# Kernel optimization log

Hardware: AMD Instinct MI355X
Metric: run time of the kernel (lower is better)

## Reference

```python
import jax, jax.numpy as jnp
import numpy as np

ND, NS, H = 100000, 10000, 128
EDD, EDS, ESD = 600000, 600000, 600000


def setup_inputs() -> dict:
    key = jax.random.key(0)
    ks = jax.random.split(key, 32)

    def n(i, shape, s=1.0):
        return jax.random.normal(ks[i], shape, dtype=jnp.float32) * s

    inp = {
        "x_drug": n(0, (ND, H)),
        "x_se": n(1, (NS, H)),
        # edge_index[0] = source node ids, edge_index[1] = destination node ids
        "ei_dd": jnp.stack([jax.random.randint(ks[2], (EDD,), 0, ND),
                             jax.random.randint(ks[3], (EDD,), 0, ND)]),
        "ei_ds": jnp.stack([jax.random.randint(ks[4], (EDS,), 0, ND),
                             jax.random.randint(ks[5], (EDS,), 0, NS)]),
        "ei_sd": jnp.stack([jax.random.randint(ks[6], (ESD,), 0, NS),
                             jax.random.randint(ks[7], (ESD,), 0, ND)]),
    }
    i = 8
    for layer in (1, 2):
        for rel in ("dd", "ds", "sd"):
            inp[f"w{layer}_{rel}_rel"] = n(i, (H, H), 0.05); i += 1
            inp[f"b{layer}_{rel}"] = jnp.zeros((H,), jnp.float32)
            inp[f"w{layer}_{rel}_root"] = n(i, (H, H), 0.05); i += 1
    inp["bn_gamma"] = jnp.ones((H,), jnp.float32)
    inp["bn_beta"] = jnp.zeros((H,), jnp.float32)
    return inp


def _gconv(x_src, x_dst, ei, w_rel, b_rel, w_root):
    # PyG GraphConv (aggr='add'): lin_rel(sum_j x_j) + lin_root(x_dst)
    agg = jax.ops.segment_sum(x_src[ei[0]], ei[1], num_segments=x_dst.shape[0])
    return agg @ w_rel.T + b_rel + x_dst @ w_root.T


def _bn(x, gamma, beta, eps=1e-5):
    # training-mode BatchNorm1d: batch stats, biased variance
    m = x.mean(axis=0)
    v = jnp.mean((x - m) ** 2, axis=0)
    return (x - m) / jnp.sqrt(v + eps) * gamma + beta


def reference(x_drug, x_se, ei_dd, ei_ds, ei_sd,
              w1_dd_rel, b1_dd, w1_dd_root,
              w1_ds_rel, b1_ds, w1_ds_root,
              w1_sd_rel, b1_sd, w1_sd_root,
              w2_dd_rel, b2_dd, w2_dd_root,
              w2_ds_rel, b2_ds, w2_ds_root,
              w2_sd_rel, b2_sd, w2_sd_root,
              bn_gamma, bn_beta):
    lrelu = jax.nn.leaky_relu  # slope 0.01, matches F.leaky_relu default
    # layer 1: HeteroConv sums per destination type
    d1 = lrelu(_gconv(x_drug, x_drug, ei_dd, w1_dd_rel, b1_dd, w1_dd_root)
               + _gconv(x_se, x_drug, ei_sd, w1_sd_rel, b1_sd, w1_sd_root))
    s1 = lrelu(_gconv(x_drug, x_se, ei_ds, w1_ds_rel, b1_ds, w1_ds_root))
    # layer 2
    d2 = lrelu(_gconv(d1, d1, ei_dd, w2_dd_rel, b2_dd, w2_dd_root)
               + _gconv(s1, d1, ei_sd, w2_sd_rel, b2_sd, w2_sd_root))
    s2 = lrelu(_gconv(d1, s1, ei_ds, w2_ds_rel, b2_ds, w2_ds_root))
    # shared BatchNorm applied per node type
    return _bn(d2, bn_gamma, bn_beta), _bn(s2, bn_gamma, bn_beta)
```

## Files before the change

### kernel.cpp

```cpp
#include <hip/hip_runtime.h>
#include <hip/hip_bf16.h>

#define H 128
#define ND 100000
#define NS 10000
#define CAPD 32
#define CAPS 128

typedef __attribute__((ext_vector_type(8))) _Float16 f16x8;
typedef __attribute__((ext_vector_type(4))) float f32x4;

__device__ inline ushort f2h(float f) {
    union { _Float16 h; ushort u; } c; c.h = (_Float16)f; return c.u;
}
__device__ inline float h2f(ushort u) {
    union { ushort u; _Float16 h; } c; c.u = u; return (float)c.h;
}

__global__ __launch_bounds__(256) void f2h_all(
    const float* __restrict__ xd, const float* __restrict__ xs,
    ushort* __restrict__ od, ushort* __restrict__ os)
{
    int i = blockIdx.x * 256 + threadIdx.x;
    const int nD = ND * H / 4;
    const int nT = (ND + NS) * H / 4;
    if (i >= nT) return;
    const float* in; ushort* out; int j;
    if (i < nD) { in = xd; out = od; j = i; }
    else        { in = xs; out = os; j = i - nD; }
    float4 v = reinterpret_cast<const float4*>(in)[j];
    ushort4 o;
    o.x = f2h(v.x); o.y = f2h(v.y); o.z = f2h(v.z); o.w = f2h(v.w);
    reinterpret_cast<ushort4*>(out)[j] = o;
}

__global__ void prep_weights(
    const float* w1ddr, const float* w1ddo, const float* w1sdr, const float* w1sdo,
    const float* w1dsr, const float* w1dso,
    const float* w2ddr, const float* w2ddo, const float* w2sdr, const float* w2sdo,
    const float* w2dsr, const float* w2dso,
    const float* b1dd, const float* b1sd, const float* b1ds,
    const float* b2dd, const float* b2sd, const float* b2ds,
    ushort* Wd1, ushort* Ws1, ushort* Wd2, ushort* Ws2, float* bias)
{
    int i = blockIdx.x * blockDim.x + threadIdx.x;
    if (i < 16384) {
        Wd1[i]           = f2h(w1ddr[i]);
        Wd1[16384 + i]   = f2h(w1sdr[i]);
        Wd1[32768 + i]   = f2h(w1ddo[i] + w1sdo[i]);
        Ws1[i]           = f2h(w1dsr[i]);
        Ws1[16384 + i]   = f2h(w1dso[i]);
        Wd2[i]           = f2h(w2ddr[i]);
        Wd2[16384 + i]   = f2h(w2sdr[i]);
        Wd2[32768 + i]   = f2h(w2ddo[i] + w2sdo[i]);
        Ws2[i]           = f2h(w2dsr[i]);
        Ws2[16384 + i]   = f2h(w2dso[i]);
    }
    if (i < H) {
        bias[i]         = b1dd[i] + b1sd[i];
        bias[H + i]     = b1ds[i];
        bias[2*H + i]   = b2dd[i] + b2sd[i];
        bias[3*H + i]   = b2ds[i];
    }
}

__global__ __launch_bounds__(256) void fill3(
    const int* __restrict__ s1, const int* __restrict__ d1, int E1, int n1, int* __restrict__ c1, int* __restrict__ o1,
    const int* __restrict__ s2, const int* __restrict__ d2, int E2, int n2, int* __restrict__ c2, ushort* __restrict__ o2,
    const int* __restrict__ s3, const int* __restrict__ d3, int E3, int n3, int* __restrict__ c3, int* __restrict__ o3,
    int g1, int g2)
{
    int pass = blockIdx.x & 7;
    int b = blockIdx.x >> 3;
    int rel;
    const int *es, *ed; int *cur; int E, n;
    if (b < g1)           { es = s1; ed = d1; cur = c1; E = E1; n = n1; rel = 0; }
    else if (b < g1 + g2) { es = s2; ed = d2; cur = c2; E = E2; n = n2; rel = 1; b -= g1; }
    else                  { es = s3; ed = d3; cur = c3; E = E3; n = n3; rel = 2; b -= g1 + g2; }
    int e = b * 256 + threadIdx.x;
    if (e >= E) return;
    int dst = ed[e];
    int lo = pass * (n >> 3);
    if (dst >= lo && dst < lo + (n >> 3)) {
        int pos = atomicAdd(&cur[dst], 1);
        if (rel == 0)      { if (pos < CAPD) o1[(size_t)dst * CAPD + pos] = es[e]; }
        else if (rel == 1) { if (pos < CAPD) o2[(size_t)dst * CAPD + pos] = (ushort)es[e]; }
        else               { if (pos < CAPS) o3[(size_t)dst * CAPS + pos] = es[e]; }
    }
}

template<typename IT>
__device__ inline uint4 agg_row(const ushort* __restrict__ src,
                                const IT* __restrict__ si, int cnt, int c)
{
    float a0 = 0.f, a1 = 0.f, a2 = 0.f, a3 = 0.f;
    float a4 = 0.f, a5 = 0.f, a6 = 0.f, a7 = 0.f;
    int p = 0;
    for (; p + 4 <= cnt; p += 4) {
        int s0 = (int)si[p], s1 = (int)si[p + 1], s2 = (int)si[p + 2], s3 = (int)si[p + 3];
        uint4 v0 = *reinterpret_cast<const uint4*>(src + (size_t)s0 * H + c * 8);
        uint4 v1 = *reinterpret_cast<const uint4*>(src + (size_t)s1 * H + c * 8);
        uint4 v2 = *reinterpret_cast<const uint4*>(src + (size_t)s2 * H + c * 8);
        uint4 v3 = *reinterpret_cast<const uint4*>(src + (size_t)s3 * H + c * 8);
        a0 += h2f((ushort)(v0.x & 0xffff)) + h2f((ushort)(v1.x & 0xffff))
            + h2f((ushort)(v2.x & 0xffff)) + h2f((ushort)(v3.x & 0xffff));
        a1 += h2f((ushort)(v0.x >> 16))    + h2f((ushort)(v1.x >> 16))
            + h2f((ushort)(v2.x >> 16))    + h2f((ushort)(v3.x >> 16));
        a2 += h2f((ushort)(v0.y & 0xffff)) + h2f((ushort)(v1.y & 0xffff))
            + h2f((ushort)(v2.y & 0xffff)) + h2f((ushort)(v3.y & 0xffff));
        a3 += h2f((ushort)(v0.y >> 16))    + h2f((ushort)(v1.y >> 16))
            + h2f((ushort)(v2.y >> 16))    + h2f((ushort)(v3.y >> 16));
        a4 += h2f((ushort)(v0.z & 0xffff)) + h2f((ushort)(v1.z & 0xffff))
            + h2f((ushort)(v2.z & 0xffff)) + h2f((ushort)(v3.z & 0xffff));
        a5 += h2f((ushort)(v0.z >> 16))    + h2f((ushort)(v1.z >> 16))
            + h2f((ushort)(v2.z >> 16))    + h2f((ushort)(v3.z >> 16));
        a6 += h2f((ushort)(v0.w & 0xffff)) + h2f((ushort)(v1.w & 0xffff))
            + h2f((ushort)(v2.w & 0xffff)) + h2f((ushort)(v3.w & 0xffff));
        a7 += h2f((ushort)(v0.w >> 16))    + h2f((ushort)(v1.w >> 16))
            + h2f((ushort)(v2.w >> 16))    + h2f((ushort)(v3.w >> 16));
    }
    for (; p < cnt; ++p) {
        int s0 = (int)si[p];
        uint4 v0 = *reinterpret_cast<const uint4*>(src + (size_t)s0 * H + c * 8);
        a0 += h2f((ushort)(v0.x & 0xffff));
        a1 += h2f((ushort)(v0.x >> 16));
        a2 += h2f((ushort)(v0.y & 0xffff));
        a3 += h2f((ushort)(v0.y >> 16));
        a4 += h2f((ushort)(v0.z & 0xffff));
        a5 += h2f((ushort)(v0.z >> 16));
        a6 += h2f((ushort)(v0.w & 0xffff));
        a7 += h2f((ushort)(v0.w >> 16));
    }
    uint4 o;
    o.x = (uint)f2h(a0) | ((uint)f2h(a1) << 16);
    o.y = (uint)f2h(a2) | ((uint)f2h(a3) << 16);
    o.z = (uint)f2h(a4) | ((uint)f2h(a5) << 16);
    o.w = (uint)f2h(a6) | ((uint)f2h(a7) << 16);
    return o;
}

__global__ __launch_bounds__(256) void agg3(
    const ushort* __restrict__ dtab, const ushort* __restrict__ stab,
    const int* __restrict__ cnt_dd, const int* __restrict__ si_dd, ushort* __restrict__ segdd,
    const int* __restrict__ cnt_sd, const ushort* __restrict__ si_sd, ushort* __restrict__ segsd,
    const int* __restrict__ cnt_ds, const int* __restrict__ si_ds, ushort* __restrict__ segds,
    int gA)
{
    int b = blockIdx.x;
    int rel; ushort* dst; int Ndst;
    if (b < gA)          { rel = 0; dst = segdd; Ndst = ND; }
    else if (b < 2 * gA) { rel = 1; dst = segsd; Ndst = ND; b -= gA; }
    else                 { rel = 2; dst = segds; Ndst = NS; b -= 2 * gA; }
    int d = b * 16 + (threadIdx.x >> 4);
    if (d >= Ndst) return;
    int c = threadIdx.x & 15;
    uint4 o;
    if (rel == 0) {
        int n = min(cnt_dd[d], CAPD);
        o = agg_row(dtab, si_dd + (size_t)d * CAPD, n, c);
    } else if (rel == 1) {
        int n = min(cnt_sd[d], CAPD);
        o = agg_row(stab, si_sd + (size_t)d * CAPD, n, c);
    } else {
        int n = min(cnt_ds[d], CAPS);
        o = agg_row(dtab, si_ds + (size_t)d * CAPS, n, c);
    }
    *reinterpret_cast<uint4*>(dst + (size_t)d * H + c * 8) = o;
}

template<bool OUTF32>
__global__ __launch_bounds__(256) void gemm_layer(
    const ushort* __restrict__ segdd, const ushort* __restrict__ segsd,
    const ushort* __restrict__ rootd, const ushort* __restrict__ Wd,
    const float* __restrict__ biasd, void* __restrict__ outd,
    const ushort* __restrict__ segds, const ushort* __restrict__ roots,
    const ushort* __restrict__ Ws, const float* __restrict__ biass,
    void* __restrict__ outs, float* __restrict__ sm, int GD)
{
    __shared__ union {
        struct { ushort Al[64][72]; ushort Bl[128][72]; } s;
        float red[2][16][128];
    } u;

    int b = blockIdx.x;
    const ushort *src0, *src1, *src2, *W; const float* bias; void* out;
    int M, nsrc, soff;
    if (b < GD) {
        src0 = segdd; src1 = segsd; src2 = rootd; W = Wd; bias = biasd;
        out = outd; M = ND; nsrc = 3; soff = 0;
    } else {
        b -= GD;
        src0 = segds; src1 = roots; src2 = nullptr; W = Ws; bias = biass;
        out = outs; M = NS; nsrc = 2; soff = 256;
    }

    const int t = threadIdx.x;
    const int wave = t >> 6;
    const int lane = t & 63;
    const int l15 = lane & 15;
    const int kreg = lane >> 4;
    const int block_row = b * 64;

    f32x4 acc[8] = {};

    for (int slot = 0; slot < nsrc; ++slot) {
        const ushort* sb = (slot == 0) ? src0 : (slot == 1) ? src1 : src2;
        #pragma unroll
        for (int half = 0; half < 2; ++half) {
            const int kc = half * 64;
            __syncthreads();
            #pragma unroll
            for (int it = 0; it < 2; ++it) {
                int c = t + it * 256;
                int row = c >> 3, part = c & 7;
                int grow = block_row + row;
                uint4 v = make_uint4(0, 0, 0, 0);
                if (grow < M)
                    v = *reinterpret_cast<const uint4*>(sb + (size_t)grow * H + kc + part * 8);
                *reinterpret_cast<uint4*>(&u.s.Al[row][part * 8]) = v;
            }
            #pragma unroll
            for (int it = 0; it < 4; ++it) {
                int c = t + it * 256;
                int row = c >> 3, part = c & 7;
                uint4 v = *reinterpret_cast<const uint4*>(W + slot * 16384 + row * 128 + kc + part * 8);
                *reinterpret_cast<uint4*>(&u.s.Bl[row][part * 8]) = v;
            }
            __syncthreads();

            #pragma unroll
            for (int kk = 0; kk < 2; ++kk) {
                f16x8 a = *reinterpret_cast<const f16x8*>(&u.s.Al[wave * 16 + l15][kk * 32 + kreg * 8]);
                #pragma unroll
                for (int n = 0; n < 8; ++n) {
                    f16x8 bb = *reinterpret_cast<const f16x8*>(&u.s.Bl[n * 16 + l15][kk * 32 + kreg * 8]);
                    acc[n] = __builtin_amdgcn_mfma_f32_16x16x32_f16(a, bb, acc[n], 0, 0, 0);
                }
            }
        }
    }

    float psum[8], psq[8];
    const int rb = block_row + wave * 16 + kreg * 4;
    #pragma unroll
    for (int n = 0; n < 8; ++n) {
        int col = n * 16 + l15;
        float bv = bias[col];
        float s = 0.f, q = 0.f;
        #pragma unroll
        for (int r = 0; r < 4; ++r) {
            int row = rb + r;
            if (row < M) {
                float v = acc[n][r] + bv;
                v = (v > 0.f) ? v : 0.01f * v;
                if (OUTF32) ((float*)out)[(size_t)row * H + col] = v;
                else        ((ushort*)out)[(size_t)row * H + col] = f2h(v);
                s += v; q += v * v;
            }
        }
        psum[n] = s; psq[n] = q;
    }

    if (OUTF32) {
        __syncthreads();
        const int w4k = wave * 4 + kreg;
        #pragma unroll
        for (int n = 0; n < 8; ++n) {
            int col = n * 16 + l15;
            u.red[0][w4k][col] = psum[n];
            u.red[1][w4k][col] = psq[n];
        }
        __syncthreads();
        if (t < 128) {
            float a = 0.f, q = 0.f;
            #pragma unroll
            for (int k = 0; k < 16; ++k) { a += u.red[0][k][t]; q += u.red[1][k][t]; }
            float* dstp = sm + (blockIdx.x & 7) * 512 + soff;
            atomicAdd(&dstp[t], a);
            atomicAdd(&dstp[H + t], q);
        }
    }
}

__global__ void bn_fold(const float* __restrict__ sm, float* __restrict__ stats)
{
    int t = blockIdx.x * 256 + threadIdx.x;
    float s = 0.f;
    #pragma unroll
    for (int k = 0; k < 8; ++k) s += sm[k * 512 + t];
    stats[t] = s;
}

__global__ __launch_bounds__(256) void bn_apply_all(
    float* __restrict__ d2, float* __restrict__ s2,
    const float* __restrict__ stats,
    const float* __restrict__ gamma, const float* __restrict__ beta)
{
    size_t i = (size_t)blockIdx.x * 256 + threadIdx.x;
    const size_t totD = (size_t)ND * (H / 4);
    const size_t totAll = totD + (size_t)NS * (H / 4);
    if (i >= totAll) return;
    float* x;
    const float* st;
    float inv_m;
    size_t j;
    if (i < totD) { x = d2; st = stats;       inv_m = 1.0f / ND; j = i; }
    else          { x = s2; st = stats + 256; inv_m = 1.0f / NS; j = i - totD; }
    int c4 = (int)(j & (H / 4 - 1)) * 4;
    float4 v = reinterpret_cast<float4*>(x)[j];
    float* vp = &v.x;
    #pragma unroll
    for (int k = 0; k < 4; ++k) {
        int c = c4 + k;
        float mean = st[c] * inv_m;
        float var = st[H + c] * inv_m - mean * mean;
        float sc = gamma[c] * rsqrtf(fmaxf(var, 0.f) + 1e-5f);
        vp[k] = (vp[k] - mean) * sc + beta[c];
    }
    reinterpret_cast<float4*>(x)[j] = v;
}

extern "C" void kernel_launch(void* const* d_in, const int* in_sizes, int n_in,
                              void* d_out, int out_size, void* d_ws, size_t ws_size,
                              hipStream_t stream)
{
    (void)n_in; (void)out_size; (void)ws_size;
    const float* x_drug = (const float*)d_in[0];
    const float* x_se   = (const float*)d_in[1];
    const int* ei_dd = (const int*)d_in[2];
    const int* ei_ds = (const int*)d_in[3];
    const int* ei_sd = (const int*)d_in[4];
    const int EDD = in_sizes[2] / 2;
    const int EDS = in_sizes[3] / 2;
    const int ESD = in_sizes[4] / 2;

    const float* w1_dd_rel  = (const float*)d_in[5];
    const float* b1_dd      = (const float*)d_in[6];
    const float* w1_dd_root = (const float*)d_in[7];
    const float* w1_ds_rel  = (const float*)d_in[8];
    const float* b1_ds      = (const float*)d_in[9];
    const float* w1_ds_root = (const float*)d_in[10];
    const float* w1_sd_rel  = (const float*)d_in[11];
    const float* b1_sd      = (const float*)d_in[12];
    const float* w1_sd_root = (const float*)d_in[13];
    const float* w2_dd_rel  = (const float*)d_in[14];
    const float* b2_dd      = (const float*)d_in[15];
    const float* w2_dd_root = (const float*)d_in[16];
    const float* w2_ds_rel  = (const float*)d_in[17];
    const float* b2_ds      = (const float*)d_in[18];
    const float* w2_ds_root = (const float*)d_in[19];
    const float* w2_sd_rel  = (const float*)d_in[20];
    const float* b2_sd      = (const float*)d_in[21];
    const float* w2_sd_root = (const float*)d_in[22];
    const float* gamma      = (const float*)d_in[23];
    const float* beta       = (const float*)d_in[24];

    ushort* xd_h  = (ushort*)d_ws;
    ushort* xs_h  = xd_h + (size_t)ND * H;
    ushort* segdd = xs_h + (size_t)NS * H;
    ushort* segsd = segdd + (size_t)ND * H;
    ushort* segds = segsd + (size_t)ND * H;
    ushort* Wd1 = segds + (size_t)NS * H;
    ushort* Ws1 = Wd1 + 3 * 16384;
    ushort* Wd2 = Ws1 + 2 * 16384;
    ushort* Ws2 = Wd2 + 3 * 16384;
    float* bias  = (float*)(Ws2 + 2 * 16384);
    float* stats = bias + 512;
    float* sm    = stats + 512;
    int* cnt_dd  = (int*)(sm + 8 * 512);
    int* cnt_sd  = cnt_dd + ND;
    int* cnt_ds  = cnt_sd + ND;
    int* si_dd   = cnt_ds + NS;
    int* si_ds   = si_dd + (size_t)ND * CAPD;
    ushort* si_sd = (ushort*)(si_ds + (size_t)NS * CAPS);

    ushort* d1h = xd_h;
    ushort* s1h = xs_h;

    float* d2 = (float*)d_out;
    float* s2 = d2 + (size_t)ND * H;

    hipMemsetAsync(sm, 0, ((size_t)8 * 512 + (size_t)(2 * ND + NS)) * sizeof(int), stream);

    prep_weights<<<64, 256, 0, stream>>>(
        w1_dd_rel, w1_dd_root, w1_sd_rel, w1_sd_root, w1_ds_rel, w1_ds_root,
        w2_dd_rel, w2_dd_root, w2_sd_rel, w2_sd_root, w2_ds_rel, w2_ds_root,
        b1_dd, b1_sd, b1_ds, b2_dd, b2_sd, b2_ds,
        Wd1, Ws1, Wd2, Ws2, bias);

    f2h_all<<<((ND + NS) * H / 4 + 255) / 256, 256, 0, stream>>>(x_drug, x_se, xd_h, xs_h);

    const int gDD = (EDD + 255) / 256, gSD = (ESD + 255) / 256, gDS = (EDS + 255) / 256;
    fill3<<<8 * (gDD + gSD + gDS), 256, 0, stream>>>(
        ei_dd, ei_dd + EDD, EDD, ND, cnt_dd, si_dd,
        ei_sd, ei_sd + ESD, ESD, ND, cnt_sd, si_sd,
        ei_ds, ei_ds + EDS, EDS, NS, cnt_ds, si_ds, gDD, gSD);

    const int gA = (ND + 15) / 16, gB = (NS + 15) / 16;
    const int GD = (ND + 63) / 64, GS = (NS + 63) / 64;

    agg3<<<2 * gA + gB, 256, 0, stream>>>(
        xd_h, xs_h,
        cnt_dd, si_dd, segdd,
        cnt_sd, si_sd, segsd,
        cnt_ds, si_ds, segds, gA);
    gemm_layer<false><<<GD + GS, 256, 0, stream>>>(
        segdd, segsd, xd_h, Wd1, bias, d1h,
        segds, xs_h, Ws1, bias + H, s1h, sm, GD);

    agg3<<<2 * gA + gB, 256, 0, stream>>>(
        d1h, s1h,
        cnt_dd, si_dd, segdd,
        cnt_sd, si_sd, segsd,
        cnt_ds, si_ds, segds, gA);
    gemm_layer<true><<<GD + GS, 256, 0, stream>>>(
        segdd, segsd, d1h, Wd2, bias + 2 * H, d2,
        segds, s1h, Ws2, bias + 3 * H, s2, sm, GD);

    bn_fold<<<2, 256, 0, stream>>>(sm, stats);
    bn_apply_all<<<((ND + NS) * (H / 4) + 255) / 256, 256, 0, stream>>>(d2, s2, stats, gamma, beta);
}
```

Before: 404.7 us.

## Load GEMM A operands directly into registers and fuse f2h into edge fill

The GEMM kernel stops staging the activation tile in LDS: each lane loads its own A fragments straight from global memory, and only the weight tile still goes through shared memory. This removes A-tile LDS traffic and shrinks shared memory use. The fp32-to-fp16 conversion kernel is merged into the CSR fill kernel to save one launch, and the aggregation tail loop is unrolled by two. The direct A loads drop the bounds check on the row index, so the last partial blocks read past M, which relies on the neighbouring buffer being mapped.

Result: faster. 377.1 us (-6.8%).

```diff
diff --git a/kernel.cpp b/kernel.cpp
--- a/kernel.cpp
+++ b/kernel.cpp
@@ -15,23 +15,6 @@
 }
 __device__ inline float h2f(ushort u) {
     union { ushort u; _Float16 h; } c; c.u = u; return (float)c.h;
-}
-
-__global__ __launch_bounds__(256) void f2h_all(
-    const float* __restrict__ xd, const float* __restrict__ xs,
-    ushort* __restrict__ od, ushort* __restrict__ os)
-{
-    int i = blockIdx.x * 256 + threadIdx.x;
-    const int nD = ND * H / 4;
-    const int nT = (ND + NS) * H / 4;
-    if (i >= nT) return;
-    const float* in; ushort* out; int j;
-    if (i < nD) { in = xd; out = od; j = i; }
-    else        { in = xs; out = os; j = i - nD; }
-    float4 v = reinterpret_cast<const float4*>(in)[j];
-    ushort4 o;
-    o.x = f2h(v.x); o.y = f2h(v.y); o.z = f2h(v.z); o.w = f2h(v.w);
-    reinterpret_cast<ushort4*>(out)[j] = o;
 }
 
 __global__ void prep_weights(
@@ -64,14 +47,30 @@
     }
 }
 
-__global__ __launch_bounds__(256) void fill3(
+__global__ __launch_bounds__(256) void fill_f2h(
+    const float* __restrict__ xd, const float* __restrict__ xs,
+    ushort* __restrict__ od, ushort* __restrict__ os, int F,
     const int* __restrict__ s1, const int* __restrict__ d1, int E1, int n1, int* __restrict__ c1, int* __restrict__ o1,
     const int* __restrict__ s2, const int* __restrict__ d2, int E2, int n2, int* __restrict__ c2, ushort* __restrict__ o2,
     const int* __restrict__ s3, const int* __restrict__ d3, int E3, int n3, int* __restrict__ c3, int* __restrict__ o3,
     int g1, int g2)
 {
+    if (blockIdx.x < F) {
+        int i = blockIdx.x * 256 + threadIdx.x;
+        const int nD = ND * H / 4;
+        const int nT = (ND + NS) * H / 4;
+        if (i >= nT) return;
+        const float* in; ushort* out; int j;
+        if (i < nD) { in = xd; out = od; j = i; }
+        else        { in = xs; out = os; j = i - nD; }
+        float4 v = reinterpret_cast<const float4*>(in)[j];
+        ushort4 o;
+        o.x = f2h(v.x); o.y = f2h(v.y); o.z = f2h(v.z); o.w = f2h(v.w);
+        reinterpret_cast<ushort4*>(out)[j] = o;
+        return;
+    }
     int pass = blockIdx.x & 7;
-    int b = blockIdx.x >> 3;
+    int b = (blockIdx.x - F) >> 3;
     int rel;
     const int *es, *ed; int *cur; int E, n;
     if (b < g1)           { es = s1; ed = d1; cur = c1; E = E1; n = n1; rel = 0; }
@@ -119,7 +118,21 @@
         a7 += h2f((ushort)(v0.w >> 16))    + h2f((ushort)(v1.w >> 16))
             + h2f((ushort)(v2.w >> 16))    + h2f((ushort)(v3.w >> 16));
     }
-    for (; p < cnt; ++p) {
+    if (p + 2 <= cnt) {
+        int s0 = (int)si[p], s1 = (int)si[p + 1];
+        uint4 v0 = *reinterpret_cast<const uint4*>(src + (size_t)s0 * H + c * 8);
+        uint4 v1 = *reinterpret_cast<const uint4*>(src + (size_t)s1 * H + c * 8);
+        a0 += h2f((ushort)(v0.x & 0xffff)) + h2f((ushort)(v1.x & 0xffff));
+        a1 += h2f((ushort)(v0.x >> 16))    + h2f((ushort)(v1.x >> 16));
+        a2 += h2f((ushort)(v0.y & 0xffff)) + h2f((ushort)(v1.y & 0xffff));
+        a3 += h2f((ushort)(v0.y >> 16))    + h2f((ushort)(v1.y >> 16));
+        a4 += h2f((ushort)(v0.z & 0xffff)) + h2f((ushort)(v1.z & 0xffff));
+        a5 += h2f((ushort)(v0.z >> 16))    + h2f((ushort)(v1.z >> 16));
+        a6 += h2f((ushort)(v0.w & 0xffff)) + h2f((ushort)(v1.w & 0xffff));
+        a7 += h2f((ushort)(v0.w >> 16))    + h2f((ushort)(v1.w >> 16));
+        p += 2;
+    }
+    if (p < cnt) {
         int s0 = (int)si[p];
         uint4 v0 = *reinterpret_cast<const uint4*>(src + (size_t)s0 * H + c * 8);
         a0 += h2f((ushort)(v0.x & 0xffff));
@@ -178,7 +191,7 @@
     void* __restrict__ outs, float* __restrict__ sm, int GD)
 {
     __shared__ union {
-        struct { ushort Al[64][72]; ushort Bl[128][72]; } s;
+        ushort Bl[128][72];
         float red[2][16][128];
     } u;
 
@@ -200,6 +213,7 @@
     const int l15 = lane & 15;
     const int kreg = lane >> 4;
     const int block_row = b * 64;
+    const int arow = block_row + wave * 16 + l15;
 
     f32x4 acc[8] = {};
 
@@ -208,34 +222,28 @@
         #pragma unroll
         for (int half = 0; half < 2; ++half) {
             const int kc = half * 64;
+            const ushort* ap = sb + (size_t)arow * H + kc + kreg * 8;
+            f16x8 a0 = *reinterpret_cast<const f16x8*>(ap);
+            f16x8 a1 = *reinterpret_cast<const f16x8*>(ap + 32);
             __syncthreads();
-            #pragma unroll
-            for (int it = 0; it < 2; ++it) {
-                int c = t + it * 256;
-                int row = c >> 3, part = c & 7;
-                int grow = block_row + row;
-                uint4 v = make_uint4(0, 0, 0, 0);
-                if (grow < M)
-                    v = *reinterpret_cast<const uint4*>(sb + (size_t)grow * H + kc + part * 8);
-                *reinterpret_cast<uint4*>(&u.s.Al[row][part * 8]) = v;
-            }
             #pragma unroll
             for (int it = 0; it < 4; ++it) {
                 int c = t + it * 256;
                 int row = c >> 3, part = c & 7;
                 uint4 v = *reinterpret_cast<const uint4*>(W + slot * 16384 + row * 128 + kc + part * 8);
-                *reinterpret_cast<uint4*>(&u.s.Bl[row][part * 8]) = v;
+                *reinterpret_cast<uint4*>(&u.Bl[row][part * 8]) = v;
             }
             __syncthreads();
 
             #pragma unroll
-            for (int kk = 0; kk < 2; ++kk) {
-                f16x8 a = *reinterpret_cast<const f16x8*>(&u.s.Al[wave * 16 + l15][kk * 32 + kreg * 8]);
-                #pragma unroll
-                for (int n = 0; n < 8; ++n) {
-                    f16x8 bb = *reinterpret_cast<const f16x8*>(&u.s.Bl[n * 16 + l15][kk * 32 + kreg * 8]);
-                    acc[n] = __builtin_amdgcn_mfma_f32_16x16x32_f16(a, bb, acc[n], 0, 0, 0);
-                }
+            for (int n = 0; n < 8; ++n) {
+                f16x8 bb = *reinterpret_cast<const f16x8*>(&u.Bl[n * 16 + l15][kreg * 8]);
+                acc[n] = __builtin_amdgcn_mfma_f32_16x16x32_f16(a0, bb, acc[n], 0, 0, 0);
+            }
+            #pragma unroll
+            for (int n = 0; n < 8; ++n) {
+                f16x8 bb = *reinterpret_cast<const f16x8*>(&u.Bl[n * 16 + l15][32 + kreg * 8]);
+                acc[n] = __builtin_amdgcn_mfma_f32_16x16x32_f16(a1, bb, acc[n], 0, 0, 0);
             }
         }
     }
@@ -388,10 +396,10 @@
         b1_dd, b1_sd, b1_ds, b2_dd, b2_sd, b2_ds,
         Wd1, Ws1, Wd2, Ws2, bias);
 
-    f2h_all<<<((ND + NS) * H / 4 + 255) / 256, 256, 0, stream>>>(x_drug, x_se, xd_h, xs_h);
-
+    const int F = ((ND + NS) * H / 4 + 255) / 256;
     const int gDD = (EDD + 255) / 256, gSD = (ESD + 255) / 256, gDS = (EDS + 255) / 256;
-    fill3<<<8 * (gDD + gSD + gDS), 256, 0, stream>>>(
+    fill_f2h<<<F + 8 * (gDD + gSD + gDS), 256, 0, stream>>>(
+        x_drug, x_se, xd_h, xs_h, F,
         ei_dd, ei_dd + EDD, EDD, ND, cnt_dd, si_dd,
         ei_sd, ei_sd + ESD, ESD, ND, cnt_sd, si_sd,
         ei_ds, ei_ds + EDS, EDS, NS, cnt_ds, si_ds, gDD, gSD);
```
